# Kernel tuning notes

Hardware: AMD Instinct MI355X
Metric: run time of the kernel (lower is better)

Reference implementation:

```python
import jax, jax.numpy as jnp
import numpy as np

D_MODEL = 1024
NUM_HEADS = 16
D_HEAD = D_MODEL // NUM_HEADS


def setup_inputs() -> dict:
    key = jax.random.key(0)
    ks = jax.random.split(key, 12)
    B, S = 2, 2048
    scale = 1.0 / np.sqrt(D_MODEL)
    inp = {
        "q": jax.random.normal(ks[0], (B, S, D_MODEL), jnp.float32),
        "k": jax.random.normal(ks[1], (B, S, D_MODEL), jnp.float32),
        "v": jax.random.normal(ks[2], (B, S, D_MODEL), jnp.float32),
        # per-head projection weights stacked: [H, d_model, d_head]
        "Wq": jax.random.normal(ks[3], (NUM_HEADS, D_MODEL, D_HEAD), jnp.float32) * scale,
        "bq": jax.random.normal(ks[4], (NUM_HEADS, D_HEAD), jnp.float32) * scale,
        "Wk": jax.random.normal(ks[5], (NUM_HEADS, D_MODEL, D_HEAD), jnp.float32) * scale,
        "bk": jax.random.normal(ks[6], (NUM_HEADS, D_HEAD), jnp.float32) * scale,
        "Wv": jax.random.normal(ks[7], (NUM_HEADS, D_MODEL, D_HEAD), jnp.float32) * scale,
        "bv": jax.random.normal(ks[8], (NUM_HEADS, D_HEAD), jnp.float32) * scale,
        "Wo": jax.random.normal(ks[9], (D_MODEL, D_MODEL), jnp.float32) * scale,
        "bo": jax.random.normal(ks[10], (D_MODEL,), jnp.float32) * scale,
    }
    return inp


def reference(q, k, v, Wq, bq, Wk, bk, Wv, bv, Wo, bo):
    # Per-head linear projections, batched over heads: [b,s,d] x [h,d,e] -> [b,h,s,e]
    qh = jnp.einsum("bsd,hde->bhse", q, Wq) + bq[None, :, None, :]
    kh = jnp.einsum("bsd,hde->bhse", k, Wk) + bk[None, :, None, :]
    vh = jnp.einsum("bsd,hde->bhse", v, Wv) + bv[None, :, None, :]
    # Scaled dot-product attention per head
    scores = jnp.einsum("bhse,bhte->bhst", qh, kh) / jnp.sqrt(jnp.asarray(D_HEAD, qh.dtype))
    weights = jax.nn.softmax(scores, axis=-1)
    out = jnp.einsum("bhst,bhte->bhse", weights, vh)
    # Concatenate heads along feature dim (head order preserved), then output linear
    B, H, S, E = out.shape
    out = out.transpose(0, 2, 1, 3).reshape(B, S, H * E)
    return out @ Wo + bo
```

## Files before the change

### kernel.cpp

```cpp
#include <hip/hip_runtime.h>
#include <cstdint>
#include <math.h>


typedef __bf16 bf16;
typedef __bf16 bf16x2 __attribute__((ext_vector_type(2)));
typedef __bf16 bf16x4 __attribute__((ext_vector_type(4)));
typedef __bf16 bf16x8 __attribute__((ext_vector_type(8)));
typedef float f32x4 __attribute__((ext_vector_type(4)));
typedef float f32x16 __attribute__((ext_vector_type(16)));
typedef unsigned u32x4 __attribute__((ext_vector_type(4)));

__device__ __forceinline__ void gl2lds16(const void* g, void* l) {
  __builtin_amdgcn_global_load_lds(
      (const __attribute__((address_space(1))) unsigned int*)g,
      (__attribute__((address_space(3))) unsigned int*)l,
      16, 0, 0);
}

__device__ __forceinline__ unsigned pkbf(float a, float b) {
  bf16x2 t;
  t[0] = (bf16)a;
  t[1] = (bf16)b;
  return __builtin_bit_cast(unsigned, t);
}

__global__ __launch_bounds__(256) void k_cvt_all(const float* __restrict__ q,
                                                 const float* __restrict__ k,
                                                 const float* __restrict__ v,
                                                 const float* __restrict__ Wq,
                                                 const float* __restrict__ Wk,
                                                 const float* __restrict__ Wv,
                                                 const float* __restrict__ Wo,
                                                 bf16* __restrict__ qkv,
                                                 bf16* __restrict__ WT,
                                                 bf16* __restrict__ WoT) {
  __shared__ float tl[64][65];
  const int bid = blockIdx.x;
  const int t = threadIdx.x;
  if (bid < 12288) {
    const int by = bid >> 12, bx = bid & 4095;
    const float* in = by == 0 ? q : (by == 1 ? k : v);
    bf16* out = qkv + (size_t)by * 4194304;
    const size_t i = ((size_t)bx * 256 + t) * 4;
    const float4 vv = *(const float4*)(in + i);
    bf16x4 o;
    o[0] = (bf16)vv.x; o[1] = (bf16)vv.y; o[2] = (bf16)vv.z; o[3] = (bf16)vv.w;
    *(bf16x4*)(out + i) = o;
  } else if (bid < 13056) {
    const int wb = bid - 12288;
    const int sel = wb >> 8;
    const int rem = wb & 255;
    const int h = rem >> 4;
    const int d0 = (rem & 15) << 6;
    const float* W = sel == 0 ? Wq : (sel == 1 ? Wk : Wv);
    const int r = t >> 2;
    const float* srcp = W + (size_t)h * 65536 + (size_t)(d0 + r) * 64 + (t & 3) * 4;
#pragma unroll
    for (int j = 0; j < 4; ++j) {
      const float4 vv = *(const float4*)(srcp + j * 16);
      const int c = (t & 3) * 4 + j * 16;
      tl[r][c] = vv.x; tl[r][c + 1] = vv.y; tl[r][c + 2] = vv.z; tl[r][c + 3] = vv.w;
    }
    __syncthreads();
    bf16* dst = WT + (size_t)sel * 1048576;
#pragma unroll
    for (int pass = 0; pass < 2; ++pass) {
      const int e = (t >> 3) + pass * 32;
      const int dd = (t & 7) * 8;
      bf16x8 o;
#pragma unroll
      for (int j = 0; j < 8; ++j) o[j] = (bf16)tl[dd + j][e];
      *(bf16x8*)(dst + (size_t)(h * 64 + e) * 1024 + d0 + dd) = o;
    }
  } else {
    const int wb = bid - 13056;
    const int n0 = (wb >> 4) << 6;
    const int k0 = (wb & 15) << 6;
    const int r = t >> 2;
    const float* srcp = Wo + (size_t)(k0 + r) * 1024 + n0 + (t & 3) * 4;
#pragma unroll
    for (int j = 0; j < 4; ++j) {
      const float4 vv = *(const float4*)(srcp + j * 16);
      const int c = (t & 3) * 4 + j * 16;
      tl[r][c] = vv.x; tl[r][c + 1] = vv.y; tl[r][c + 2] = vv.z; tl[r][c + 3] = vv.w;
    }
    __syncthreads();
#pragma unroll
    for (int pass = 0; pass < 2; ++pass) {
      const int e = (t >> 3) + pass * 32;
      const int dd = (t & 7) * 8;
      bf16x8 o;
#pragma unroll
      for (int j = 0; j < 8; ++j) o[j] = (bf16)tl[dd + j][e];
      *(bf16x8*)(WoT + (size_t)(n0 + e) * 1024 + k0 + dd) = o;
    }
  }
}

__global__ __launch_bounds__(512, 4) void k_gemm_qkv(const bf16* __restrict__ Abase,
                                                     const bf16* __restrict__ Bt,
                                                     const float* __restrict__ bq,
                                                     const float* __restrict__ bk,
                                                     const float* __restrict__ bv,
                                                     bf16* __restrict__ Qh,
                                                     bf16* __restrict__ Kh,
                                                     bf16* __restrict__ Vt) {
  __shared__ __align__(16) bf16 lds[32768];
  const int t = threadIdx.x;
  const int lane = t & 63;
  const int lane15 = lane & 15;
  const int quad = lane >> 4;
  const int w = t >> 6;
  const int wm = w >> 2;
  const int wn = w & 3;

  const int bid = blockIdx.x;
  const int wgid = (bid & 7) * 96 + (bid >> 3);
  const int nb = wgid % 24;
  const int mb = wgid / 24;
  const int sel = nb >> 3;
  const int nbl = (nb & 7) << 7;

  const bf16* A = Abase + (size_t)sel * 4194304;
  const int sr = t >> 3;
  const int sc = ((t & 7) - sr) & 7;
  const bf16* AgS = A + (size_t)(mb * 128 + sr) * 1024 + sc * 8;
  const bf16* BgS = Bt + (size_t)(nb * 128 + sr) * 1024 + sc * 8;

#define QKV_STAGE(kt, d)                           \
  do {                                             \
    const int _k = (kt) * 64;                      \
    bf16* _la = lds + (d) * 8192 + t * 8;          \
    bf16* _lb = lds + 16384 + (d) * 8192 + t * 8;  \
    gl2lds16(AgS + _k, _la);                       \
    gl2lds16(AgS + 65536 + _k, _la + 4096);        \
    gl2lds16(BgS + _k, _lb);                       \
    gl2lds16(BgS + 65536 + _k, _lb + 4096);        \
  } while (0)

  f32x4 acc[4][2] = {};
  const int arow = (wm * 64 + lane15) * 64;
  const int brow = 16384 + (wn * 32 + lane15) * 64;

  QKV_STAGE(0, 0);
  QKV_STAGE(1, 1);

#pragma unroll 2
  for (int kt = 0; kt < 16; ++kt) {
    const int d = kt & 1;
    if (kt == 15)
      asm volatile("s_waitcnt vmcnt(0)" ::: "memory");
    else
      asm volatile("s_waitcnt vmcnt(4)" ::: "memory");
    __builtin_amdgcn_s_barrier();
    const int base = d * 8192;
    {
      const int p = ((quad + lane15) & 7) * 8;
      bf16x8 af[4], bfr[2];
#pragma unroll
      for (int i = 0; i < 4; ++i)
        af[i] = *(const bf16x8*)(lds + base + arow + i * 1024 + p);
#pragma unroll
      for (int j = 0; j < 2; ++j)
        bfr[j] = *(const bf16x8*)(lds + base + brow + j * 1024 + p);
      __builtin_amdgcn_s_setprio(1);
#pragma unroll
      for (int i = 0; i < 4; ++i)
#pragma unroll
        for (int j = 0; j < 2; ++j)
          acc[i][j] = __builtin_amdgcn_mfma_f32_16x16x32_bf16(af[i], bfr[j], acc[i][j], 0, 0, 0);
      __builtin_amdgcn_s_setprio(0);
    }
    {
      const int p = ((quad + 4 + lane15) & 7) * 8;
      bf16x8 ag[4], bg[2];
#pragma unroll
      for (int i = 0; i < 4; ++i)
        ag[i] = *(const bf16x8*)(lds + base + arow + i * 1024 + p);
#pragma unroll
      for (int j = 0; j < 2; ++j)
        bg[j] = *(const bf16x8*)(lds + base + brow + j * 1024 + p);
      asm volatile("s_waitcnt lgkmcnt(0)" ::: "memory");
      __builtin_amdgcn_s_barrier();
      if (kt < 14) QKV_STAGE(kt + 2, d);
      __builtin_amdgcn_s_setprio(1);
#pragma unroll
      for (int i = 0; i < 4; ++i)
#pragma unroll
        for (int j = 0; j < 2; ++j)
          acc[i][j] = __builtin_amdgcn_mfma_f32_16x16x32_bf16(ag[i], bg[j], acc[i][j], 0, 0, 0);
      __builtin_amdgcn_s_setprio(0);
    }
  }
#undef QKV_STAGE

  const float scale = sel == 0 ? 0.18033688011112042f : 1.0f;
  const float* bias = sel == 0 ? bq : (sel == 1 ? bk : bv);
  const int mbase = mb * 128 + wm * 64;
  if (sel < 2) {
    bf16* outp = sel == 0 ? Qh : Kh;
#pragma unroll
    for (int j = 0; j < 2; ++j) {
      const int n = nbl + wn * 32 + j * 16 + lane15;
      const float bvl = bias[n];
      const int h = n >> 6, e = n & 63;
#pragma unroll
      for (int i = 0; i < 4; ++i) {
#pragma unroll
        for (int r = 0; r < 4; ++r) {
          const int m = mbase + i * 16 + quad * 4 + r;
          const float vv = (acc[i][j][r] + bvl) * scale;
          const int b = m >> 11, s = m & 2047;
          outp[(size_t)(b * 16 + h) * 131072 + s * 64 + e] = (bf16)vv;
        }
      }
    }
  } else {
#pragma unroll
    for (int j = 0; j < 2; ++j) {
      const int n = nbl + wn * 32 + j * 16 + lane15;
      const float bvl = bias[n];
      const int h = n >> 6, e = n & 63;
#pragma unroll
      for (int i = 0; i < 4; ++i) {
        const int m = mbase + i * 16 + quad * 4;
        const int b = m >> 11, s = m & 2047;
        bf16x4 o;
#pragma unroll
        for (int r = 0; r < 4; ++r) o[r] = (bf16)(acc[i][j][r] + bvl);
        *(bf16x4*)(Vt + (size_t)(b * 16 + h) * 131072 + e * 2048 + s) = o;
      }
    }
  }
}

__global__ __launch_bounds__(512, 4) void k_attn(const bf16* __restrict__ Qh,
                                                 const bf16* __restrict__ Kh,
                                                 const bf16* __restrict__ Vt,
                                                 bf16* __restrict__ attn) {
  __shared__ __align__(16) bf16 lds[32768];
  const int t = threadIdx.x;
  const int w = t >> 6;
  const int lane = t & 63;
  const int lane31 = lane & 31;
  const int hi = lane >> 5;
  const int bh = blockIdx.y;
  const bf16* Qp = Qh + (size_t)bh * 131072;
  const bf16* Kp = Kh + (size_t)bh * 131072;
  const bf16* Vp = Vt + (size_t)bh * 131072;
  const int h = w >> 2;
  const int q0 = blockIdx.x * 128 + (w & 3) * 32;

  bf16x8 aq[4];
#pragma unroll
  for (int kc = 0; kc < 4; ++kc)
    aq[kc] = *(const bf16x8*)(Qp + (size_t)(q0 + lane31) * 64 + kc * 16 + hi * 8);

  int raddr[4];
#pragma unroll
  for (int cc = 0; cc < 4; ++cc)
    raddr[cc] = lane31 * 64 + (((cc * 2 + hi + lane31) & 7) << 3);

  const bf16* kg[2];
  const bf16* vg[2];
  int kdst[2], vdst[2];
#pragma unroll
  for (int i = 0; i < 2; ++i) {
    const int cid = w * 2 + i;
    const int half = cid >> 3;
    const int sl = ((cid & 7) << 6) + lane;
    const int row = sl >> 3;
    const int c = ((sl & 7) - row) & 7;
    kg[i] = Kp + ((size_t)(half << 10) + row) * 64 + c * 8;
    vg[i] = Vp + (size_t)row * 2048 + (half << 10) + c * 8;
    kdst[i] = (half << 14) + ((cid & 7) << 9);
    vdst[i] = kdst[i] + 8192;
  }

  f32x16 O[2] = {};
  float l_ = 0.f;

#pragma unroll
  for (int i = 0; i < 2; ++i) {
    gl2lds16(kg[i], lds + kdst[i]);
    gl2lds16(vg[i], lds + vdst[i]);
  }

#pragma unroll 2
  for (int it = 0; it < 16; ++it) {
    const int bufo = (it & 1) << 12;
    __syncthreads();
    if (it + 1 < 16) {
      const int po = bufo ^ 4096;
#pragma unroll
      for (int i = 0; i < 2; ++i) {
        gl2lds16(kg[i] + (size_t)(it + 1) * 4096, lds + kdst[i] + po);
        gl2lds16(vg[i] + (it + 1) * 64, lds + vdst[i] + po);
      }
    }

    const bf16* Kl = lds + (h << 14) + bufo;
    f32x16 sa = {}, sb = {};
#pragma unroll
    for (int kc = 0; kc < 4; ++kc) {
      bf16x8 a0 = *(const bf16x8*)(Kl + raddr[kc]);
      bf16x8 a1 = *(const bf16x8*)(Kl + 2048 + raddr[kc]);
      sa = __builtin_amdgcn_mfma_f32_32x32x16_bf16(a0, aq[kc], sa, 0, 0, 0);
      sb = __builtin_amdgcn_mfma_f32_32x32x16_bf16(a1, aq[kc], sb, 0, 0, 0);
    }

    float rs = 0.f;
#pragma unroll
    for (int r = 0; r < 16; ++r) {
      sa[r] = __builtin_amdgcn_exp2f(sa[r]);
      sb[r] = __builtin_amdgcn_exp2f(sb[r]);
      rs += sa[r] + sb[r];
    }
    rs += __shfl_xor(rs, 32);
    l_ += rs;

    unsigned P2[2][8];
#pragma unroll
    for (int kq = 0; kq < 8; ++kq) {
      P2[0][kq] = pkbf(sa[2 * kq], sa[2 * kq + 1]);
      P2[1][kq] = pkbf(sb[2 * kq], sb[2 * kq + 1]);
    }

    const bf16* Vl = lds + (h << 14) + 8192 + bufo;
#pragma unroll
    for (int kk = 0; kk < 4; ++kk) {
      const int kmt = kk >> 1, kc = kk & 1;
      const unsigned mineA = hi ? P2[kmt][4 * kc + 2] : P2[kmt][4 * kc];
      const unsigned mineB = hi ? P2[kmt][4 * kc + 3] : P2[kmt][4 * kc + 1];
      const unsigned sendA = hi ? P2[kmt][4 * kc] : P2[kmt][4 * kc + 2];
      const unsigned sendB = hi ? P2[kmt][4 * kc + 1] : P2[kmt][4 * kc + 3];
      const unsigned ZA = (unsigned)__shfl_xor((int)sendA, 32);
      const unsigned ZB = (unsigned)__shfl_xor((int)sendB, 32);
      u32x4 bpi;
      bpi[0] = hi ? ZA : mineA;
      bpi[1] = hi ? ZB : mineB;
      bpi[2] = hi ? mineA : ZA;
      bpi[3] = hi ? mineB : ZB;
      const bf16x8 bp = __builtin_bit_cast(bf16x8, bpi);
#pragma unroll
      for (int emt = 0; emt < 2; ++emt) {
        bf16x8 av = *(const bf16x8*)(Vl + emt * 2048 + raddr[kk]);
        O[emt] = __builtin_amdgcn_mfma_f32_32x32x16_bf16(av, bp, O[emt], 0, 0, 0);
      }
    }
  }

  float* fl = (float*)lds;
  __syncthreads();
  if (w >= 4) {
#pragma unroll
    for (int emt = 0; emt < 2; ++emt)
#pragma unroll
      for (int r = 0; r < 16; ++r)
        fl[(w - 4) * 2048 + (emt * 16 + r) * 64 + lane] = O[emt][r];
    if (lane < 32) fl[8192 + (w - 4) * 32 + lane] = l_;
  }
  __syncthreads();
  if (w < 4) {
#pragma unroll
    for (int emt = 0; emt < 2; ++emt)
#pragma unroll
      for (int r = 0; r < 16; ++r)
        O[emt][r] += fl[w * 2048 + (emt * 16 + r) * 64 + lane];
    const float lsum = l_ + fl[8192 + w * 32 + lane31];
    const float inv = 1.0f / lsum;

    const int b = bh >> 4, hh = bh & 15;
    const int q = q0 + lane31;
    bf16* orow = attn + (size_t)(b * 2048 + q) * 1024 + hh * 64;
#pragma unroll
    for (int emt = 0; emt < 2; ++emt) {
#pragma unroll
      for (int kp = 0; kp < 8; ++kp) {
        const int r = 2 * kp;
        const int e0 = emt * 32 + (r & 3) + 8 * (kp >> 1) + 4 * hi;
        bf16x2 pr;
        pr[0] = (bf16)(O[emt][r] * inv);
        pr[1] = (bf16)(O[emt][r + 1] * inv);
        *(bf16x2*)(orow + e0) = pr;
      }
    }
  }
}

__global__ __launch_bounds__(256, 3) void k_gemm2(const bf16* __restrict__ A,
                                                  const bf16* __restrict__ Bt,
                                                  const float* __restrict__ bias,
                                                  float* __restrict__ outp) {
  __shared__ __align__(16) bf16 lds[24576];
  const int t = threadIdx.x;
  const int lane = t & 63;
  const int lane15 = lane & 15;
  const int quad = lane >> 4;
  const int w = t >> 6;
  const int wm = w >> 1;
  const int wn = w & 1;

  const int bid = blockIdx.x;
  const int wgid = (bid & 7) * 64 + (bid >> 3);
  const int nb = wgid & 15;
  const int mb = wgid >> 4;

  const int sr = t >> 3;
  const int sc = ((t & 7) - sr) & 7;
  const bf16* AgS = A + (size_t)(mb * 128 + sr) * 1024 + sc * 8;
  const bf16* BgS = Bt + (size_t)(nb * 64 + sr) * 1024 + sc * 8;

#define G2_STAGE(kt, d)                            \
  do {                                             \
    const int _k = (kt) * 64;                      \
    bf16* _la = lds + (d) * 8192 + t * 8;          \
    bf16* _lb = lds + 16384 + (d) * 4096 + t * 8;  \
    gl2lds16(AgS + _k, _la);                       \
    gl2lds16(AgS + 32768 + _k, _la + 2048);        \
    gl2lds16(AgS + 65536 + _k, _la + 4096);        \
    gl2lds16(AgS + 98304 + _k, _la + 6144);        \
    gl2lds16(BgS + _k, _lb);                       \
    gl2lds16(BgS + 32768 + _k, _lb + 2048);        \
  } while (0)

  f32x4 acc[4][2] = {};
  const int arow = (wm * 64 + lane15) * 64;
  const int brow = 16384 + (wn * 32 + lane15) * 64;

  G2_STAGE(0, 0);
  G2_STAGE(1, 1);

#pragma unroll 2
  for (int kt = 0; kt < 16; ++kt) {
    const int d = kt & 1;
    if (kt == 15)
      asm volatile("s_waitcnt vmcnt(0)" ::: "memory");
    else
      asm volatile("s_waitcnt vmcnt(6)" ::: "memory");
    __builtin_amdgcn_s_barrier();
    const int baseA = d * 8192;
    const int baseB = d * 4096;
    {
      const int p = ((quad + lane15) & 7) * 8;
      bf16x8 af[4], bfr[2];
#pragma unroll
      for (int i = 0; i < 4; ++i)
        af[i] = *(const bf16x8*)(lds + baseA + arow + i * 1024 + p);
#pragma unroll
      for (int j = 0; j < 2; ++j)
        bfr[j] = *(const bf16x8*)(lds + baseB + brow + j * 1024 + p);
      __builtin_amdgcn_s_setprio(1);
#pragma unroll
      for (int i = 0; i < 4; ++i)
#pragma unroll
        for (int j = 0; j < 2; ++j)
          acc[i][j] = __builtin_amdgcn_mfma_f32_16x16x32_bf16(af[i], bfr[j], acc[i][j], 0, 0, 0);
      __builtin_amdgcn_s_setprio(0);
    }
    {
      const int p = ((quad + 4 + lane15) & 7) * 8;
      bf16x8 ag[4], bg[2];
#pragma unroll
      for (int i = 0; i < 4; ++i)
        ag[i] = *(const bf16x8*)(lds + baseA + arow + i * 1024 + p);
#pragma unroll
      for (int j = 0; j < 2; ++j)
        bg[j] = *(const bf16x8*)(lds + baseB + brow + j * 1024 + p);
      asm volatile("s_waitcnt lgkmcnt(0)" ::: "memory");
      __builtin_amdgcn_s_barrier();
      if (kt < 14) G2_STAGE(kt + 2, d);
      __builtin_amdgcn_s_setprio(1);
#pragma unroll
      for (int i = 0; i < 4; ++i)
#pragma unroll
        for (int j = 0; j < 2; ++j)
          acc[i][j] = __builtin_amdgcn_mfma_f32_16x16x32_bf16(ag[i], bg[j], acc[i][j], 0, 0, 0);
      __builtin_amdgcn_s_setprio(0);
    }
  }
#undef G2_STAGE

  const int mbase = mb * 128 + wm * 64;
  const int nbase = nb * 64 + wn * 32;
#pragma unroll
  for (int j = 0; j < 2; ++j) {
    const int n = nbase + j * 16 + lane15;
    const float bv = bias[n];
#pragma unroll
    for (int i = 0; i < 4; ++i) {
#pragma unroll
      for (int r = 0; r < 4; ++r) {
        const int m = mbase + i * 16 + quad * 4 + r;
        outp[(size_t)m * 1024 + n] = acc[i][j][r] + bv;
      }
    }
  }
}

extern "C" void kernel_launch(void* const* d_in, const int* in_sizes, int n_in,
                              void* d_out, int out_size, void* d_ws, size_t ws_size,
                              hipStream_t stream) {
  (void)in_sizes; (void)n_in; (void)out_size; (void)ws_size;
  const float* q = (const float*)d_in[0];
  const float* k = (const float*)d_in[1];
  const float* v = (const float*)d_in[2];
  const float* Wq = (const float*)d_in[3];
  const float* bq = (const float*)d_in[4];
  const float* Wk = (const float*)d_in[5];
  const float* bk = (const float*)d_in[6];
  const float* Wv = (const float*)d_in[7];
  const float* bv = (const float*)d_in[8];
  const float* Wo = (const float*)d_in[9];
  const float* bo = (const float*)d_in[10];

  bf16* ws = (bf16*)d_ws;
  bf16* qkv = ws;
  bf16* WqkvT = qkv + 12582912;
  bf16* WoT = WqkvT + 3145728;
  bf16* Qh = WoT + 1048576;
  bf16* Kh = Qh + 4194304;
  bf16* Vt = Kh + 4194304;
  bf16* attnb = Vt + 4194304;

  k_cvt_all<<<13312, 256, 0, stream>>>(q, k, v, Wq, Wk, Wv, Wo, qkv, WqkvT, WoT);
  k_gemm_qkv<<<768, 512, 0, stream>>>(qkv, WqkvT, bq, bk, bv, Qh, Kh, Vt);
  k_attn<<<dim3(16, 32), 512, 0, stream>>>(Qh, Kh, Vt, attnb);
  k_gemm2<<<512, 256, 0, stream>>>(attnb, WoT, bo, (float*)d_out);
}
```

Measured before the change: 215.4 us.

## Prefetch two K/V stages ahead with vmcnt waits and XCD-aware block mapping

The attention kernel now issues K/V tile loads two iterations ahead and waits with explicit vmcnt counters plus raw barriers, instead of a full __syncthreads before a one-ahead prefetch. A second barrier at the end of each iteration protects the buffer about to be overwritten. The grid is flattened to 1D and remapped so blocks on the same XCD share the same (batch, head), which should improve L2 reuse of K/V. This adds an extra barrier per iteration and depends on the hand-tuned wait counts being correct.

```diff
diff --git a/kernel.cpp b/kernel.cpp
--- a/kernel.cpp
+++ b/kernel.cpp
@@ -245,12 +245,18 @@
   const int lane = t & 63;
   const int lane31 = lane & 31;
   const int hi = lane >> 5;
-  const int bh = blockIdx.y;
+
+  const int bid = blockIdx.x;
+  const int xcd = bid & 7;
+  const int loc = bid >> 3;
+  const int bh = xcd * 4 + (loc >> 4);
+  const int qt = loc & 15;
+
   const bf16* Qp = Qh + (size_t)bh * 131072;
   const bf16* Kp = Kh + (size_t)bh * 131072;
   const bf16* Vp = Vt + (size_t)bh * 131072;
   const int h = w >> 2;
-  const int q0 = blockIdx.x * 128 + (w & 3) * 32;
+  const int q0 = qt * 128 + (w & 3) * 32;
 
   bf16x8 aq[4];
 #pragma unroll
@@ -278,27 +284,29 @@
     vdst[i] = kdst[i] + 8192;
   }
 
+#define ATTN_STAGE(it)                                          \
+  do {                                                          \
+    const int _po = ((it) & 1) << 12;                           \
+    gl2lds16(kg[0] + (size_t)(it) * 4096, lds + kdst[0] + _po); \
+    gl2lds16(vg[0] + (it) * 64, lds + vdst[0] + _po);           \
+    gl2lds16(kg[1] + (size_t)(it) * 4096, lds + kdst[1] + _po); \
+    gl2lds16(vg[1] + (it) * 64, lds + vdst[1] + _po);           \
+  } while (0)
+
   f32x16 O[2] = {};
   float l_ = 0.f;
 
-#pragma unroll
-  for (int i = 0; i < 2; ++i) {
-    gl2lds16(kg[i], lds + kdst[i]);
-    gl2lds16(vg[i], lds + vdst[i]);
-  }
+  ATTN_STAGE(0);
+  ATTN_STAGE(1);
 
 #pragma unroll 2
   for (int it = 0; it < 16; ++it) {
     const int bufo = (it & 1) << 12;
-    __syncthreads();
-    if (it + 1 < 16) {
-      const int po = bufo ^ 4096;
-#pragma unroll
-      for (int i = 0; i < 2; ++i) {
-        gl2lds16(kg[i] + (size_t)(it + 1) * 4096, lds + kdst[i] + po);
-        gl2lds16(vg[i] + (it + 1) * 64, lds + vdst[i] + po);
-      }
-    }
+    if (it == 15)
+      asm volatile("s_waitcnt vmcnt(0)" ::: "memory");
+    else
+      asm volatile("s_waitcnt vmcnt(4)" ::: "memory");
+    __builtin_amdgcn_s_barrier();
 
     const bf16* Kl = lds + (h << 14) + bufo;
     f32x16 sa = {}, sb = {};
@@ -349,7 +357,12 @@
         O[emt] = __builtin_amdgcn_mfma_f32_32x32x16_bf16(av, bp, O[emt], 0, 0, 0);
       }
     }
-  }
+
+    asm volatile("s_waitcnt lgkmcnt(0)" ::: "memory");
+    __builtin_amdgcn_s_barrier();
+    if (it < 14) ATTN_STAGE(it + 2);
+  }
+#undef ATTN_STAGE
 
   float* fl = (float*)lds;
   __syncthreads();
@@ -526,6 +539,6 @@
 
   k_cvt_all<<<13312, 256, 0, stream>>>(q, k, v, Wq, Wk, Wv, Wo, qkv, WqkvT, WoT);
   k_gemm_qkv<<<768, 512, 0, stream>>>(qkv, WqkvT, bq, bk, bv, Qh, Kh, Vt);
-  k_attn<<<dim3(16, 32), 512, 0, stream>>>(Qh, Kh, Vt, attnb);
+  k_attn<<<512, 512, 0, stream>>>(Qh, Kh, Vt, attnb);
   k_gemm2<<<512, 256, 0, stream>>>(attnb, WoT, bo, (float*)d_out);
 }
```

Result: no change. 216.1 us (+0.3%).
